# Kernel optimization log

Measured on AMD Instinct MI355X. Metric: run time of the kernel, lower is better.

The kernel has to match this reference:

```python
import jax, jax.numpy as jnp
import numpy as np

HIDDEN = 1024
OUT = 16

def setup_inputs() -> dict:
    key = jax.random.key(0)
    ks = jax.random.split(key, 12)
    bs, hl, hf = 256, 256, 32
    T, ad = 64, 16
    flat = hl * hf
    s = lambda fi, fo: 1.0 / np.sqrt(fi)
    return {
        "history": jax.random.normal(ks[0], (bs, hl, hf), jnp.float32),
        "action": jax.random.normal(ks[1], (bs, T, ad), jnp.float32),
        # carry-init Dense layers (c and h)
        "Wc": jax.random.normal(ks[2], (flat, HIDDEN), jnp.float32) * s(flat, HIDDEN),
        "bc": jnp.zeros((HIDDEN,), jnp.float32),
        "Wh": jax.random.normal(ks[3], (flat, HIDDEN), jnp.float32) * s(flat, HIDDEN),
        "bh": jnp.zeros((HIDDEN,), jnp.float32),
        # LSTM cell: gates ordered [i, f, g, o]; input dense has no bias (flax LSTMCell)
        "Wi": jax.random.normal(ks[4], (ad, 4 * HIDDEN), jnp.float32) * s(ad, HIDDEN),
        "Wr": jax.random.normal(ks[5], (HIDDEN, 4 * HIDDEN), jnp.float32) * s(HIDDEN, HIDDEN),
        "bg": jnp.zeros((4 * HIDDEN,), jnp.float32),
        # output projection
        "Wo": jax.random.normal(ks[6], (HIDDEN, OUT), jnp.float32) * s(HIDDEN, OUT),
        "bo": jnp.zeros((OUT,), jnp.float32),
    }


def reference(history, action, Wc, bc, Wh, bh, Wi, Wr, bg, Wo, bo):
    bs = history.shape[0]
    flat = history.reshape(bs, -1)
    c0 = jax.nn.relu(flat @ Wc + bc)  # [bs, H]
    h0 = jax.nn.relu(flat @ Wh + bh)  # [bs, H]

    # precompute input contribution to gates for all steps: [T, bs, 4H]
    xg = jnp.einsum('bta,ag->tbg', action, Wi)

    def step(carry, xg_t):
        c, h = carry
        g = xg_t + h @ Wr + bg  # [bs, 4H]
        i, f, gg, o = jnp.split(g, 4, axis=-1)
        c = jax.nn.sigmoid(f) * c + jax.nn.sigmoid(i) * jnp.tanh(gg)
        h = jax.nn.sigmoid(o) * jnp.tanh(c)
        return (c, h), h

    _, hs = jax.lax.scan(step, (c0, h0), xg)  # hs: [T, bs, H]
    x = jnp.transpose(hs, (1, 0, 2))  # [bs, T, H]
    # Dropout is deterministic (identity)
    return x @ Wo + bo  # [bs, T, OUT]
```

## Files before the change

### kernel.cpp

```cpp
#include <hip/hip_runtime.h>
#include <math.h>

#define BS      256
#define FLAT    8192
#define H       1024
#define G4      4096
#define T_STEPS 64
#define AD      16
#define NOUT    16

typedef __attribute__((ext_vector_type(8))) short    bf16x8;
typedef __attribute__((ext_vector_type(4))) float    f32x4;
typedef __attribute__((ext_vector_type(8))) unsigned short u16x8;
typedef __attribute__((ext_vector_type(4))) unsigned short u16x4;

__device__ __forceinline__ float sigf(float x) { return 1.0f / (1.0f + __expf(-x)); }
__device__ __forceinline__ float tanh_fast(float x) {
    float a = fabsf(x);
    float e = __expf(-2.0f * a);
    float r = (1.0f - e) / (1.0f + e);
    return copysignf(r, x);
}
__device__ __forceinline__ unsigned short f2bf(float x) {
    unsigned int u = __float_as_uint(x);
    unsigned int r = (u + 0x7FFFu + ((u >> 16) & 1u)) >> 16;
    return (unsigned short)r;
}
__device__ __forceinline__ float bf2f(unsigned short u) {
    return __uint_as_float(((unsigned int)u) << 16);
}

#define OFF_WRP  (1u<<20)
#define OFF_WIP  (OFF_WRP + (8u<<20))
#define OFF_BGP  (OFF_WIP + (256u<<10))
#define OFF_HPA  (OFF_BGP + (16u<<10))
#define OFF_HPB  (OFF_HPA + (512u<<10))
#define OFF_HS   (OFF_HPB + (512u<<10))
#define OFF_AHP  (OFF_HS + (32u<<20))
#define OFF_AXP  (OFF_AHP + (4u<<20))
#define OFF_PART (OFF_AXP + (1u<<20))

__global__ __launch_bounds__(256) void pack_wr(const float* __restrict__ Wr,
                                               unsigned short* __restrict__ Wp)
{
    int g  = blockIdx.x * 256 + threadIdx.x;
    int l  = g & 63;
    int nt = (g >> 6) & 3;
    int kc = (g >> 8) & 31;
    int nb = g >> 13;
    int col   = nt * 1024 + nb * 16 + (l & 15);
    int kbase = kc * 32 + (l >> 4) * 8;
    u16x8 o;
    #pragma unroll
    for (int i = 0; i < 8; ++i)
        o[i] = f2bf(Wr[(size_t)(kbase + i) * G4 + col]);
    *(u16x8*)&Wp[(size_t)g * 8] = o;
}

__global__ __launch_bounds__(256) void pack_wi(const float* __restrict__ Wi,
                                               unsigned short* __restrict__ Wp)
{
    int g  = blockIdx.x * 256 + threadIdx.x;
    int l  = g & 63;
    int nt = (g >> 6) & 3;
    int nb = g >> 8;
    int col   = nt * 1024 + nb * 16 + (l & 15);
    int kbase = (l >> 4) * 8;
    u16x8 o;
    #pragma unroll
    for (int i = 0; i < 8; ++i)
        o[i] = (kbase + i < AD) ? f2bf(Wi[(size_t)(kbase + i) * G4 + col]) : (unsigned short)0;
    *(u16x8*)&Wp[(size_t)g * 8] = o;
}

__global__ __launch_bounds__(256) void pack_bg(const float* __restrict__ bg,
                                               float* __restrict__ bgp)
{
    int t = blockIdx.x * 256 + threadIdx.x;
    int jj = t & 15, nt = (t >> 4) & 3, nb = t >> 6;
    bgp[t] = bg[nt * 1024 + nb * 16 + jj];
}

__global__ __launch_bounds__(256) void pack_hist(const float* __restrict__ hist,
                                                 unsigned short* __restrict__ Ap)
{
    int g  = blockIdx.x * 256 + threadIdx.x;
    int l  = g & 63;
    int kc = (g >> 6) & 255;
    int mb = g >> 14;
    const float* src = hist + (size_t)(mb * 16 + (l & 15)) * FLAT + kc * 32 + (l >> 4) * 8;
    float4 v0 = *(const float4*)src;
    float4 v1 = *(const float4*)(src + 4);
    u16x8 o;
    o[0]=f2bf(v0.x); o[1]=f2bf(v0.y); o[2]=f2bf(v0.z); o[3]=f2bf(v0.w);
    o[4]=f2bf(v1.x); o[5]=f2bf(v1.y); o[6]=f2bf(v1.z); o[7]=f2bf(v1.w);
    *(u16x8*)&Ap[(size_t)g * 8] = o;
}

__global__ __launch_bounds__(256) void pack_wb(const float* __restrict__ Wc,
                                               const float* __restrict__ Wh,
                                               unsigned short* __restrict__ Bp)
{
    int g  = blockIdx.x * 256 + threadIdx.x;
    int l  = g & 63;
    int kc = (g >> 6) & 255;
    int nb = g >> 14;
    const float* src = (nb & 64) ? Wh : Wc;
    int n = (nb & 63) * 16 + (l & 15);
    int k = kc * 32 + (l >> 4) * 8;
    u16x8 o;
    #pragma unroll
    for (int i = 0; i < 8; ++i)
        o[i] = f2bf(src[(size_t)(k + i) * H + n]);
    *(u16x8*)&Bp[(size_t)g * 8] = o;
}

__global__ __launch_bounds__(256) void pack_act(const float* __restrict__ act,
                                                unsigned short* __restrict__ Axp)
{
    int g = blockIdx.x * 256 + threadIdx.x;
    int l = g & 63;
    int q = (g >> 6) & 15;
    int t = g >> 10;
    int row = q * 16 + (l & 15);
    int kb  = (l >> 4) * 8;
    u16x8 o;
    if (kb < AD) {
        const float* src = act + ((size_t)row * T_STEPS + t) * AD + kb;
        float4 v0 = *(const float4*)src;
        float4 v1 = *(const float4*)(src + 4);
        o[0]=f2bf(v0.x); o[1]=f2bf(v0.y); o[2]=f2bf(v0.z); o[3]=f2bf(v0.w);
        o[4]=f2bf(v1.x); o[5]=f2bf(v1.y); o[6]=f2bf(v1.z); o[7]=f2bf(v1.w);
    } else {
        o = (u16x8){0,0,0,0,0,0,0,0};
    }
    *(u16x8*)&Axp[(size_t)g * 8] = o;
}

__global__ __launch_bounds__(256) void init_gemm_mfma(
    const unsigned short* __restrict__ Ap,
    const unsigned short* __restrict__ Bp,
    float* __restrict__ part)
{
    const int wg  = blockIdx.x;
    const int mb  = wg & 3;
    const int nbl = (wg >> 2) & 15;
    const int ks  = wg >> 6;
    const int tid = threadIdx.x;
    const int wv  = tid >> 6;
    const int l   = tid & 63;
    const int wm  = wv & 1;
    const int wn  = wv >> 1;

    const bf16x8* AV = (const bf16x8*)Ap;
    const bf16x8* BV = (const bf16x8*)Bp;
    const int am0 = mb * 4 + wm * 2;
    const int bn0 = nbl * 8 + wn * 4;
    const bf16x8* A0 = AV + (size_t)am0 * 16384 + l;
    const bf16x8* A1 = A0 + 16384;
    const bf16x8* B0 = BV + (size_t)bn0 * 16384 + l;
    const bf16x8* B1 = B0 + 16384;
    const bf16x8* B2 = B1 + 16384;
    const bf16x8* B3 = B2 + 16384;

    const int k0 = ks * 64;
    f32x4 acc[2][4];
    #pragma unroll
    for (int m = 0; m < 2; ++m)
        #pragma unroll
        for (int n = 0; n < 4; ++n)
            acc[m][n] = (f32x4){0.f, 0.f, 0.f, 0.f};

    bf16x8 a0 = A0[(size_t)k0 * 64], a1 = A1[(size_t)k0 * 64];
    bf16x8 b0 = B0[(size_t)k0 * 64], b1 = B1[(size_t)k0 * 64];
    bf16x8 b2 = B2[(size_t)k0 * 64], b3 = B3[(size_t)k0 * 64];

    for (int kc = k0; kc < k0 + 64; ++kc) {
        bf16x8 na0, na1, nb0, nb1, nb2, nb3;
        const bool more = (kc + 1) < k0 + 64;
        if (more) {
            size_t off = (size_t)(kc + 1) * 64;
            na0 = A0[off]; na1 = A1[off];
            nb0 = B0[off]; nb1 = B1[off]; nb2 = B2[off]; nb3 = B3[off];
        }
        acc[0][0] = __builtin_amdgcn_mfma_f32_16x16x32_bf16(a0, b0, acc[0][0], 0, 0, 0);
        acc[0][1] = __builtin_amdgcn_mfma_f32_16x16x32_bf16(a0, b1, acc[0][1], 0, 0, 0);
        acc[0][2] = __builtin_amdgcn_mfma_f32_16x16x32_bf16(a0, b2, acc[0][2], 0, 0, 0);
        acc[0][3] = __builtin_amdgcn_mfma_f32_16x16x32_bf16(a0, b3, acc[0][3], 0, 0, 0);
        acc[1][0] = __builtin_amdgcn_mfma_f32_16x16x32_bf16(a1, b0, acc[1][0], 0, 0, 0);
        acc[1][1] = __builtin_amdgcn_mfma_f32_16x16x32_bf16(a1, b1, acc[1][1], 0, 0, 0);
        acc[1][2] = __builtin_amdgcn_mfma_f32_16x16x32_bf16(a1, b2, acc[1][2], 0, 0, 0);
        acc[1][3] = __builtin_amdgcn_mfma_f32_16x16x32_bf16(a1, b3, acc[1][3], 0, 0, 0);
        if (more) { a0 = na0; a1 = na1; b0 = nb0; b1 = nb1; b2 = nb2; b3 = nb3; }
    }

    const int rbase = mb * 64 + wm * 32 + (l >> 4) * 4;
    const int cbase = nbl * 128 + wn * 64 + (l & 15);
    float* pdst = part + (size_t)ks * (BS * 2048);
    #pragma unroll
    for (int m = 0; m < 2; ++m)
        #pragma unroll
        for (int n = 0; n < 4; ++n)
            #pragma unroll
            for (int r = 0; r < 4; ++r)
                pdst[(size_t)(rbase + m * 16 + r) * 2048 + cbase + n * 16] = acc[m][n][r];
}

__global__ __launch_bounds__(256) void init_reduce(
    const float* __restrict__ part,
    const float* __restrict__ bc, const float* __restrict__ bh,
    float* __restrict__ cbuf, unsigned short* __restrict__ hp0)
{
    int e = blockIdx.x * 256 + threadIdx.x;
    int row = e >> 11, col = e & 2047;
    float s = (col < 1024) ? bc[col] : bh[col - 1024];
    #pragma unroll
    for (int ks = 0; ks < 4; ++ks)
        s += part[(size_t)ks * (BS * 2048) + e];
    s = fmaxf(s, 0.f);
    if (col < 1024) {
        cbuf[(size_t)row * H + col] = s;
    } else {
        int hid = col - 1024;
        int off = (row >> 6) * 65536 + (hid >> 5) * 2048 + ((row >> 4) & 3) * 512
                + ((((hid >> 3) & 3) << 4) + (row & 15)) * 8 + (hid & 7);
        hp0[off] = f2bf(s);
    }
}

__global__ __launch_bounds__(256) void lstm_step(
    const unsigned short* __restrict__ Axp,
    const unsigned short* __restrict__ Wip,
    const unsigned short* __restrict__ Wrp,
    const float* __restrict__ bgp,
    const unsigned short* __restrict__ Aprev,
    unsigned short* __restrict__ Anext,
    float* __restrict__ cbuf,
    unsigned short* __restrict__ hs_t,
    int t)
{
    __shared__ __align__(16) unsigned short sB[2][4096];

    const int tid = threadIdx.x;
    const int wg  = blockIdx.x;
    const int mb  = wg >> 6;
    const int nb  = wg & 63;
    const int wv  = tid >> 6;
    const int l   = tid & 63;

    const u16x8* Bsrc = (const u16x8*)(Wrp + (size_t)nb * 65536);
    {
        u16x8 s0 = Bsrc[tid], s1 = Bsrc[256 + tid];
        *(u16x8*)&sB[0][tid * 8]         = s0;
        *(u16x8*)&sB[0][(256 + tid) * 8] = s1;
    }
    u16x8 stg0 = Bsrc[512 + tid];
    u16x8 stg1 = Bsrc[768 + tid];

    const bf16x8* Asrc = ((const bf16x8*)Aprev) + mb * 8192 + wv * 64 + l;
    bf16x8 aE0 = Asrc[0],   aE1 = Asrc[256];
    bf16x8 aO0 = Asrc[512], aO1 = Asrc[768];

    f32x4 acc[4];
    {
        const bf16x8* WiB = ((const bf16x8*)Wip) + nb * 256;
        bf16x8 wb0 = WiB[0 * 64 + l], wb1 = WiB[1 * 64 + l],
               wb2 = WiB[2 * 64 + l], wb3 = WiB[3 * 64 + l];
        float g0 = bgp[nb * 64 +  0 + (l & 15)];
        float g1 = bgp[nb * 64 + 16 + (l & 15)];
        float g2 = bgp[nb * 64 + 32 + (l & 15)];
        float g3 = bgp[nb * 64 + 48 + (l & 15)];
        acc[0] = (f32x4){ g0, g0, g0, g0 };
        acc[1] = (f32x4){ g1, g1, g1, g1 };
        acc[2] = (f32x4){ g2, g2, g2, g2 };
        acc[3] = (f32x4){ g3, g3, g3, g3 };

        bf16x8 aa = *(((const bf16x8*)Axp) + ((size_t)t * 16 + mb * 4 + wv) * 64 + l);
        acc[0] = __builtin_amdgcn_mfma_f32_16x16x32_bf16(aa, wb0, acc[0], 0, 0, 0);
        acc[1] = __builtin_amdgcn_mfma_f32_16x16x32_bf16(aa, wb1, acc[1], 0, 0, 0);
        acc[2] = __builtin_amdgcn_mfma_f32_16x16x32_bf16(aa, wb2, acc[2], 0, 0, 0);
        acc[3] = __builtin_amdgcn_mfma_f32_16x16x32_bf16(aa, wb3, acc[3], 0, 0, 0);
    }
    __syncthreads();

    #define CHUNK_BODY(C, CB, AX0, AX1)                                             \
    {                                                                               \
        bf16x8 n0, n1;                                                              \
        if ((C) < 14) { n0 = Asrc[(2*(C)+4) * 256]; n1 = Asrc[(2*(C)+5) * 256]; }   \
        bf16x8 bf00 = *(const bf16x8*)&sB[CB][(0 * 64 + l) * 8];                    \
        bf16x8 bf01 = *(const bf16x8*)&sB[CB][(1 * 64 + l) * 8];                    \
        bf16x8 bf02 = *(const bf16x8*)&sB[CB][(2 * 64 + l) * 8];                    \
        bf16x8 bf03 = *(const bf16x8*)&sB[CB][(3 * 64 + l) * 8];                    \
        bf16x8 bf10 = *(const bf16x8*)&sB[CB][(4 * 64 + l) * 8];                    \
        bf16x8 bf11 = *(const bf16x8*)&sB[CB][(5 * 64 + l) * 8];                    \
        bf16x8 bf12 = *(const bf16x8*)&sB[CB][(6 * 64 + l) * 8];                    \
        bf16x8 bf13 = *(const bf16x8*)&sB[CB][(7 * 64 + l) * 8];                    \
        if ((C) < 15) {                                                             \
            *(u16x8*)&sB[(CB) ^ 1][tid * 8]         = stg0;                         \
            *(u16x8*)&sB[(CB) ^ 1][(256 + tid) * 8] = stg1;                         \
        }                                                                           \
        if ((C) < 14) {                                                             \
            stg0 = Bsrc[((C) + 2) * 512 + tid];                                     \
            stg1 = Bsrc[((C) + 2) * 512 + 256 + tid];                               \
        }                                                                           \
        acc[0] = __builtin_amdgcn_mfma_f32_16x16x32_bf16(AX0, bf00, acc[0], 0,0,0); \
        acc[1] = __builtin_amdgcn_mfma_f32_16x16x32_bf16(AX0, bf01, acc[1], 0,0,0); \
        acc[2] = __builtin_amdgcn_mfma_f32_16x16x32_bf16(AX0, bf02, acc[2], 0,0,0); \
        acc[3] = __builtin_amdgcn_mfma_f32_16x16x32_bf16(AX0, bf03, acc[3], 0,0,0); \
        acc[0] = __builtin_amdgcn_mfma_f32_16x16x32_bf16(AX1, bf10, acc[0], 0,0,0); \
        acc[1] = __builtin_amdgcn_mfma_f32_16x16x32_bf16(AX1, bf11, acc[1], 0,0,0); \
        acc[2] = __builtin_amdgcn_mfma_f32_16x16x32_bf16(AX1, bf12, acc[2], 0,0,0); \
        acc[3] = __builtin_amdgcn_mfma_f32_16x16x32_bf16(AX1, bf13, acc[3], 0,0,0); \
        if ((C) < 14) { AX0 = n0; AX1 = n1; }                                       \
        __syncthreads();                                                            \
    }

    for (int it = 0; it < 8; ++it) {
        const int c0 = 2 * it;
        CHUNK_BODY(c0,     0, aE0, aE1)
        CHUNK_BODY(c0 + 1, 1, aO0, aO1)
    }
    #undef CHUNK_BODY

    {
        const int jj   = l & 15;
        const int hid  = nb * 16 + jj;
        const int rowb = mb * 64 + wv * 16 + (l >> 4) * 4;
        const int kc   = nb >> 1;
        const int hgrp = ((nb & 1) << 1) | (jj >> 3);
        const int ii   = jj & 7;
        #pragma unroll
        for (int r = 0; r < 4; ++r) {
            int row = rowb + r;
            float gi = acc[0][r], gf = acc[1][r], gg = acc[2][r], go = acc[3][r];
            size_t off = (size_t)row * H + hid;
            float cv = sigf(gf) * cbuf[off] + sigf(gi) * tanh_fast(gg);
            cbuf[off] = cv;
            float hv = sigf(go) * tanh_fast(cv);
            unsigned short hb = f2bf(hv);
            hs_t[off] = hb;
            size_t poff = (size_t)mb * 65536 + kc * 2048 + wv * 512
                        + (hgrp * 16 + (row & 15)) * 8 + ii;
            Anext[poff] = hb;
        }
    }
}

__global__ __launch_bounds__(256) void out_proj(
    const unsigned short* __restrict__ hs,
    const float* __restrict__ Wo,
    const float* __restrict__ bo,
    float* __restrict__ out)
{
    __shared__ float sWo[H * NOUT];
    const int tid = threadIdx.x;
    for (int idx = tid; idx < H * NOUT; idx += 256) sWo[idx] = Wo[idx];
    __syncthreads();

    const int o  = tid & 15;
    const int pl = tid >> 4;
    const float bias = bo[o];
    #pragma unroll
    for (int pass = 0; pass < 4; ++pass) {
        const int pair = blockIdx.x * 64 + pass * 16 + pl;
        const int b = pair >> 6;
        const int t = pair & 63;
        const unsigned short* hrow = hs + ((size_t)t * BS + b) * H;
        float acc = bias;
        for (int k = 0; k < H; k += 8) {
            u16x8 u = *(const u16x8*)&hrow[k];
            #pragma unroll
            for (int j = 0; j < 8; ++j)
                acc = fmaf(bf2f(u[j]), sWo[(k + j) * 16 + o], acc);
        }
        out[(size_t)pair * 16 + o] = acc;
    }
}

extern "C" void kernel_launch(void* const* d_in, const int* in_sizes, int n_in,
                              void* d_out, int out_size, void* d_ws, size_t ws_size,
                              hipStream_t stream)
{
    const float* hist = (const float*)d_in[0];
    const float* act  = (const float*)d_in[1];
    const float* Wc   = (const float*)d_in[2];
    const float* bc   = (const float*)d_in[3];
    const float* Wh   = (const float*)d_in[4];
    const float* bh   = (const float*)d_in[5];
    const float* Wi   = (const float*)d_in[6];
    const float* Wr   = (const float*)d_in[7];
    const float* bg   = (const float*)d_in[8];
    const float* Wo   = (const float*)d_in[9];
    const float* bo   = (const float*)d_in[10];
    float* out = (float*)d_out;

    char* W = (char*)d_ws;
    float*          cbuf = (float*)W;
    unsigned short* Wrp  = (unsigned short*)(W + OFF_WRP);
    unsigned short* Wip  = (unsigned short*)(W + OFF_WIP);
    float*          bgp  = (float*)(W + OFF_BGP);
    unsigned short* hpA  = (unsigned short*)(W + OFF_HPA);
    unsigned short* hpB  = (unsigned short*)(W + OFF_HPB);
    unsigned short* hs   = (unsigned short*)(W + OFF_HS);
    unsigned short* Bwp  = (unsigned short*)(W + OFF_HS);
    unsigned short* Ahp  = (unsigned short*)(W + OFF_AHP);
    unsigned short* Axp  = (unsigned short*)(W + OFF_AXP);
    float*          part = (float*)(W + OFF_PART);

    pack_wr  <<<dim3(2048), dim3(256), 0, stream>>>(Wr, Wrp);
    pack_wi  <<<dim3(64),   dim3(256), 0, stream>>>(Wi, Wip);
    pack_bg  <<<dim3(16),   dim3(256), 0, stream>>>(bg, bgp);
    pack_hist<<<dim3(1024), dim3(256), 0, stream>>>(hist, Ahp);
    pack_wb  <<<dim3(8192), dim3(256), 0, stream>>>(Wc, Wh, Bwp);
    pack_act <<<dim3(256),  dim3(256), 0, stream>>>(act, Axp);

    init_gemm_mfma<<<dim3(256), dim3(256), 0, stream>>>(Ahp, Bwp, part);
    init_reduce  <<<dim3(2048), dim3(256), 0, stream>>>(part, bc, bh, cbuf, hpA);

    for (int t = 0; t < T_STEPS; ++t) {
        const unsigned short* Ap = (t & 1) ? hpB : hpA;
        unsigned short*       An = (t & 1) ? hpA : hpB;
        lstm_step<<<dim3(256), dim3(256), 0, stream>>>(
            Axp, Wip, Wrp, bgp, Ap, An, cbuf, hs + (size_t)t * BS * H, t);
    }

    out_proj<<<dim3(256), dim3(256), 0, stream>>>(hs, Wo, bo, out);
}
```

Before: 729.5 us.

## Fuse LSTM steps into persistent kernel with grid barrier and MFMA output projection

Replaces 64 per-step kernel launches with one persistent kernel of 256 workgroups that loops over time steps. Steps are separated by an atomic grid barrier, and the cell state stays in registers across steps. The output projection is rewritten to use bf16 MFMA with a packed Wo instead of scalar FMAs. This removes per-step launch overhead and the cbuf global round-trips. In exchange it depends on all 256 blocks being co-resident, and the spin barrier adds its own latency.

```diff
diff --git a/kernel.cpp b/kernel.cpp
--- a/kernel.cpp
+++ b/kernel.cpp
@@ -12,7 +12,6 @@
 typedef __attribute__((ext_vector_type(8))) short    bf16x8;
 typedef __attribute__((ext_vector_type(4))) float    f32x4;
 typedef __attribute__((ext_vector_type(8))) unsigned short u16x8;
-typedef __attribute__((ext_vector_type(4))) unsigned short u16x4;
 
 __device__ __forceinline__ float sigf(float x) { return 1.0f / (1.0f + __expf(-x)); }
 __device__ __forceinline__ float tanh_fast(float x) {
@@ -25,9 +24,6 @@
     unsigned int u = __float_as_uint(x);
     unsigned int r = (u + 0x7FFFu + ((u >> 16) & 1u)) >> 16;
     return (unsigned short)r;
-}
-__device__ __forceinline__ float bf2f(unsigned short u) {
-    return __uint_as_float(((unsigned int)u) << 16);
 }
 
 #define OFF_WRP  (1u<<20)
@@ -39,6 +35,8 @@
 #define OFF_AHP  (OFF_HS + (32u<<20))
 #define OFF_AXP  (OFF_AHP + (4u<<20))
 #define OFF_PART (OFF_AXP + (1u<<20))
+#define OFF_WOP  (OFF_PART + (8u<<20))
+#define OFF_BAR  (OFF_WOP + (64u<<10))
 
 __global__ __launch_bounds__(256) void pack_wr(const float* __restrict__ Wr,
                                                unsigned short* __restrict__ Wp)
@@ -135,6 +133,23 @@
         o = (u16x8){0,0,0,0,0,0,0,0};
     }
     *(u16x8*)&Axp[(size_t)g * 8] = o;
+}
+
+__global__ __launch_bounds__(256) void pack_wo(const float* __restrict__ Wo,
+                                               unsigned short* __restrict__ Wop)
+{
+    int g = blockIdx.x * 256 + threadIdx.x;
+    int l = g & 63;
+    int kc = g >> 6;
+    u16x8 o;
+    #pragma unroll
+    for (int i = 0; i < 8; ++i)
+        o[i] = f2bf(Wo[(size_t)(kc * 32 + (l >> 4) * 8 + i) * NOUT + (l & 15)]);
+    *(u16x8*)&Wop[(size_t)g * 8] = o;
+}
+
+__global__ void bar_init(unsigned int* bar) {
+    if (threadIdx.x == 0 && blockIdx.x == 0) *bar = 0u;
 }
 
 __global__ __launch_bounds__(256) void init_gemm_mfma(
@@ -228,16 +243,16 @@
     }
 }
 
-__global__ __launch_bounds__(256) void lstm_step(
+__global__ __launch_bounds__(256) void lstm_scan_persist(
     const unsigned short* __restrict__ Axp,
     const unsigned short* __restrict__ Wip,
     const unsigned short* __restrict__ Wrp,
     const float* __restrict__ bgp,
-    const unsigned short* __restrict__ Aprev,
-    unsigned short* __restrict__ Anext,
-    float* __restrict__ cbuf,
-    unsigned short* __restrict__ hs_t,
-    int t)
+    const float* __restrict__ cbuf,
+    unsigned short* __restrict__ hpA,
+    unsigned short* __restrict__ hpB,
+    unsigned short* __restrict__ hs,
+    unsigned int*   __restrict__ bar)
 {
     __shared__ __align__(16) unsigned short sB[2][4096];
 
@@ -248,133 +263,169 @@
     const int wv  = tid >> 6;
     const int l   = tid & 63;
 
+    const int jj   = l & 15;
+    const int hid  = nb * 16 + jj;
+    const int rowb = mb * 64 + wv * 16 + (l >> 4) * 4;
+    const int kcp  = nb >> 1;
+    const int hgrp = ((nb & 1) << 1) | (jj >> 3);
+    const int ii   = jj & 7;
+
+    float c_reg[4];
+    #pragma unroll
+    for (int r = 0; r < 4; ++r)
+        c_reg[r] = cbuf[(size_t)(rowb + r) * H + hid];
+
+    const bf16x8* WiB = ((const bf16x8*)Wip) + nb * 256;
+    const bf16x8 wb0 = WiB[0 * 64 + l], wb1 = WiB[1 * 64 + l],
+                 wb2 = WiB[2 * 64 + l], wb3 = WiB[3 * 64 + l];
+    const float g0 = bgp[nb * 64 +  0 + jj];
+    const float g1 = bgp[nb * 64 + 16 + jj];
+    const float g2 = bgp[nb * 64 + 32 + jj];
+    const float g3 = bgp[nb * 64 + 48 + jj];
+
     const u16x8* Bsrc = (const u16x8*)(Wrp + (size_t)nb * 65536);
-    {
-        u16x8 s0 = Bsrc[tid], s1 = Bsrc[256 + tid];
-        *(u16x8*)&sB[0][tid * 8]         = s0;
-        *(u16x8*)&sB[0][(256 + tid) * 8] = s1;
-    }
-    u16x8 stg0 = Bsrc[512 + tid];
-    u16x8 stg1 = Bsrc[768 + tid];
-
-    const bf16x8* Asrc = ((const bf16x8*)Aprev) + mb * 8192 + wv * 64 + l;
-    bf16x8 aE0 = Asrc[0],   aE1 = Asrc[256];
-    bf16x8 aO0 = Asrc[512], aO1 = Asrc[768];
-
-    f32x4 acc[4];
-    {
-        const bf16x8* WiB = ((const bf16x8*)Wip) + nb * 256;
-        bf16x8 wb0 = WiB[0 * 64 + l], wb1 = WiB[1 * 64 + l],
-               wb2 = WiB[2 * 64 + l], wb3 = WiB[3 * 64 + l];
-        float g0 = bgp[nb * 64 +  0 + (l & 15)];
-        float g1 = bgp[nb * 64 + 16 + (l & 15)];
-        float g2 = bgp[nb * 64 + 32 + (l & 15)];
-        float g3 = bgp[nb * 64 + 48 + (l & 15)];
+
+    #pragma unroll 1
+    for (int t = 0; t < T_STEPS; ++t) {
+        const unsigned short* Ap = (t & 1) ? hpB : hpA;
+        unsigned short*       An = (t & 1) ? hpA : hpB;
+        unsigned short*       hs_t = hs + (size_t)t * (BS * H);
+
+        {
+            u16x8 s0 = Bsrc[tid], s1 = Bsrc[256 + tid];
+            *(u16x8*)&sB[0][tid * 8]         = s0;
+            *(u16x8*)&sB[0][(256 + tid) * 8] = s1;
+        }
+        u16x8 stg0 = Bsrc[512 + tid];
+        u16x8 stg1 = Bsrc[768 + tid];
+
+        const bf16x8* Asrc = ((const bf16x8*)Ap) + mb * 8192 + wv * 64 + l;
+        bf16x8 aE0 = Asrc[0],   aE1 = Asrc[256];
+        bf16x8 aO0 = Asrc[512], aO1 = Asrc[768];
+
+        f32x4 acc[4];
         acc[0] = (f32x4){ g0, g0, g0, g0 };
         acc[1] = (f32x4){ g1, g1, g1, g1 };
         acc[2] = (f32x4){ g2, g2, g2, g2 };
         acc[3] = (f32x4){ g3, g3, g3, g3 };
-
-        bf16x8 aa = *(((const bf16x8*)Axp) + ((size_t)t * 16 + mb * 4 + wv) * 64 + l);
-        acc[0] = __builtin_amdgcn_mfma_f32_16x16x32_bf16(aa, wb0, acc[0], 0, 0, 0);
-        acc[1] = __builtin_amdgcn_mfma_f32_16x16x32_bf16(aa, wb1, acc[1], 0, 0, 0);
-        acc[2] = __builtin_amdgcn_mfma_f32_16x16x32_bf16(aa, wb2, acc[2], 0, 0, 0);
-        acc[3] = __builtin_amdgcn_mfma_f32_16x16x32_bf16(aa, wb3, acc[3], 0, 0, 0);
-    }
-    __syncthreads();
-
-    #define CHUNK_BODY(C, CB, AX0, AX1)                                             \
-    {                                                                               \
-        bf16x8 n0, n1;                                                              \
-        if ((C) < 14) { n0 = Asrc[(2*(C)+4) * 256]; n1 = Asrc[(2*(C)+5) * 256]; }   \
-        bf16x8 bf00 = *(const bf16x8*)&sB[CB][(0 * 64 + l) * 8];                    \
-        bf16x8 bf01 = *(const bf16x8*)&sB[CB][(1 * 64 + l) * 8];                    \
-        bf16x8 bf02 = *(const bf16x8*)&sB[CB][(2 * 64 + l) * 8];                    \
-        bf16x8 bf03 = *(const bf16x8*)&sB[CB][(3 * 64 + l) * 8];                    \
-        bf16x8 bf10 = *(const bf16x8*)&sB[CB][(4 * 64 + l) * 8];                    \
-        bf16x8 bf11 = *(const bf16x8*)&sB[CB][(5 * 64 + l) * 8];                    \
-        bf16x8 bf12 = *(const bf16x8*)&sB[CB][(6 * 64 + l) * 8];                    \
-        bf16x8 bf13 = *(const bf16x8*)&sB[CB][(7 * 64 + l) * 8];                    \
-        if ((C) < 15) {                                                             \
-            *(u16x8*)&sB[(CB) ^ 1][tid * 8]         = stg0;                         \
-            *(u16x8*)&sB[(CB) ^ 1][(256 + tid) * 8] = stg1;                         \
-        }                                                                           \
-        if ((C) < 14) {                                                             \
-            stg0 = Bsrc[((C) + 2) * 512 + tid];                                     \
-            stg1 = Bsrc[((C) + 2) * 512 + 256 + tid];                               \
-        }                                                                           \
-        acc[0] = __builtin_amdgcn_mfma_f32_16x16x32_bf16(AX0, bf00, acc[0], 0,0,0); \
-        acc[1] = __builtin_amdgcn_mfma_f32_16x16x32_bf16(AX0, bf01, acc[1], 0,0,0); \
-        acc[2] = __builtin_amdgcn_mfma_f32_16x16x32_bf16(AX0, bf02, acc[2], 0,0,0); \
-        acc[3] = __builtin_amdgcn_mfma_f32_16x16x32_bf16(AX0, bf03, acc[3], 0,0,0); \
-        acc[0] = __builtin_amdgcn_mfma_f32_16x16x32_bf16(AX1, bf10, acc[0], 0,0,0); \
-        acc[1] = __builtin_amdgcn_mfma_f32_16x16x32_bf16(AX1, bf11, acc[1], 0,0,0); \
-        acc[2] = __builtin_amdgcn_mfma_f32_16x16x32_bf16(AX1, bf12, acc[2], 0,0,0); \
-        acc[3] = __builtin_amdgcn_mfma_f32_16x16x32_bf16(AX1, bf13, acc[3], 0,0,0); \
-        if ((C) < 14) { AX0 = n0; AX1 = n1; }                                       \
-        __syncthreads();                                                            \
-    }
-
-    for (int it = 0; it < 8; ++it) {
-        const int c0 = 2 * it;
-        CHUNK_BODY(c0,     0, aE0, aE1)
-        CHUNK_BODY(c0 + 1, 1, aO0, aO1)
-    }
-    #undef CHUNK_BODY
-
-    {
-        const int jj   = l & 15;
-        const int hid  = nb * 16 + jj;
-        const int rowb = mb * 64 + wv * 16 + (l >> 4) * 4;
-        const int kc   = nb >> 1;
-        const int hgrp = ((nb & 1) << 1) | (jj >> 3);
-        const int ii   = jj & 7;
+        {
+            bf16x8 aa = *(((const bf16x8*)Axp) + ((size_t)t * 16 + mb * 4 + wv) * 64 + l);
+            acc[0] = __builtin_amdgcn_mfma_f32_16x16x32_bf16(aa, wb0, acc[0], 0, 0, 0);
+            acc[1] = __builtin_amdgcn_mfma_f32_16x16x32_bf16(aa, wb1, acc[1], 0, 0, 0);
+            acc[2] = __builtin_amdgcn_mfma_f32_16x16x32_bf16(aa, wb2, acc[2], 0, 0, 0);
+            acc[3] = __builtin_amdgcn_mfma_f32_16x16x32_bf16(aa, wb3, acc[3], 0, 0, 0);
+        }
+        __syncthreads();
+
+        #define CHUNK_BODY(C, CB, AX0, AX1)                                             \
+        {                                                                               \
+            bf16x8 n0, n1;                                                              \
+            if ((C) < 14) { n0 = Asrc[(2*(C)+4) * 256]; n1 = Asrc[(2*(C)+5) * 256]; }   \
+            bf16x8 bf00 = *(const bf16x8*)&sB[CB][(0 * 64 + l) * 8];                    \
+            bf16x8 bf01 = *(const bf16x8*)&sB[CB][(1 * 64 + l) * 8];                    \
+            bf16x8 bf02 = *(const bf16x8*)&sB[CB][(2 * 64 + l) * 8];                    \
+            bf16x8 bf03 = *(const bf16x8*)&sB[CB][(3 * 64 + l) * 8];                    \
+            bf16x8 bf10 = *(const bf16x8*)&sB[CB][(4 * 64 + l) * 8];                    \
+            bf16x8 bf11 = *(const bf16x8*)&sB[CB][(5 * 64 + l) * 8];                    \
+            bf16x8 bf12 = *(const bf16x8*)&sB[CB][(6 * 64 + l) * 8];                    \
+            bf16x8 bf13 = *(const bf16x8*)&sB[CB][(7 * 64 + l) * 8];                    \
+            if ((C) < 15) {                                                             \
+                *(u16x8*)&sB[(CB) ^ 1][tid * 8]         = stg0;                         \
+                *(u16x8*)&sB[(CB) ^ 1][(256 + tid) * 8] = stg1;                         \
+            }                                                                           \
+            if ((C) < 14) {                                                             \
+                stg0 = Bsrc[((C) + 2) * 512 + tid];                                     \
+                stg1 = Bsrc[((C) + 2) * 512 + 256 + tid];                               \
+            }                                                                           \
+            acc[0] = __builtin_amdgcn_mfma_f32_16x16x32_bf16(AX0, bf00, acc[0], 0,0,0); \
+            acc[1] = __builtin_amdgcn_mfma_f32_16x16x32_bf16(AX0, bf01, acc[1], 0,0,0); \
+            acc[2] = __builtin_amdgcn_mfma_f32_16x16x32_bf16(AX0, bf02, acc[2], 0,0,0); \
+            acc[3] = __builtin_amdgcn_mfma_f32_16x16x32_bf16(AX0, bf03, acc[3], 0,0,0); \
+            acc[0] = __builtin_amdgcn_mfma_f32_16x16x32_bf16(AX1, bf10, acc[0], 0,0,0); \
+            acc[1] = __builtin_amdgcn_mfma_f32_16x16x32_bf16(AX1, bf11, acc[1], 0,0,0); \
+            acc[2] = __builtin_amdgcn_mfma_f32_16x16x32_bf16(AX1, bf12, acc[2], 0,0,0); \
+            acc[3] = __builtin_amdgcn_mfma_f32_16x16x32_bf16(AX1, bf13, acc[3], 0,0,0); \
+            if ((C) < 14) { AX0 = n0; AX1 = n1; }                                       \
+            __syncthreads();                                                            \
+        }
+
+        for (int it = 0; it < 8; ++it) {
+            const int c0 = 2 * it;
+            CHUNK_BODY(c0,     0, aE0, aE1)
+            CHUNK_BODY(c0 + 1, 1, aO0, aO1)
+        }
+        #undef CHUNK_BODY
+
         #pragma unroll
         for (int r = 0; r < 4; ++r) {
             int row = rowb + r;
             float gi = acc[0][r], gf = acc[1][r], gg = acc[2][r], go = acc[3][r];
-            size_t off = (size_t)row * H + hid;
-            float cv = sigf(gf) * cbuf[off] + sigf(gi) * tanh_fast(gg);
-            cbuf[off] = cv;
+            float cv = sigf(gf) * c_reg[r] + sigf(gi) * tanh_fast(gg);
+            c_reg[r] = cv;
             float hv = sigf(go) * tanh_fast(cv);
             unsigned short hb = f2bf(hv);
-            hs_t[off] = hb;
-            size_t poff = (size_t)mb * 65536 + kc * 2048 + wv * 512
+            hs_t[(size_t)row * H + hid] = hb;
+            size_t poff = (size_t)mb * 65536 + kcp * 2048 + wv * 512
                         + (hgrp * 16 + (row & 15)) * 8 + ii;
-            Anext[poff] = hb;
-        }
-    }
-}
-
-__global__ __launch_bounds__(256) void out_proj(
+            An[poff] = hb;
+        }
+
+        if (t < T_STEPS - 1) {
+            __syncthreads();
+            if (tid == 0) {
+                __hip_atomic_fetch_add(bar, 1u, __ATOMIC_RELEASE,
+                                       __HIP_MEMORY_SCOPE_AGENT);
+                const unsigned int target = 256u * (unsigned int)(t + 1);
+                while (__hip_atomic_load(bar, __ATOMIC_ACQUIRE,
+                                         __HIP_MEMORY_SCOPE_AGENT) < target) {
+                    __builtin_amdgcn_s_sleep(1);
+                }
+            }
+            __syncthreads();
+            __builtin_amdgcn_fence(__ATOMIC_ACQUIRE, "agent");
+        }
+    }
+}
+
+__global__ __launch_bounds__(256) void out_gemm(
     const unsigned short* __restrict__ hs,
-    const float* __restrict__ Wo,
+    const unsigned short* __restrict__ Wop,
     const float* __restrict__ bo,
     float* __restrict__ out)
 {
-    __shared__ float sWo[H * NOUT];
+    __shared__ __align__(16) unsigned short sWo[32 * 64 * 8];
     const int tid = threadIdx.x;
-    for (int idx = tid; idx < H * NOUT; idx += 256) sWo[idx] = Wo[idx];
+    #pragma unroll
+    for (int u = 0; u < 8; ++u) {
+        int idx = u * 256 + tid;
+        *(u16x8*)&sWo[idx * 8] = ((const u16x8*)Wop)[idx];
+    }
     __syncthreads();
 
-    const int o  = tid & 15;
-    const int pl = tid >> 4;
-    const float bias = bo[o];
-    #pragma unroll
-    for (int pass = 0; pass < 4; ++pass) {
-        const int pair = blockIdx.x * 64 + pass * 16 + pl;
-        const int b = pair >> 6;
-        const int t = pair & 63;
-        const unsigned short* hrow = hs + ((size_t)t * BS + b) * H;
-        float acc = bias;
-        for (int k = 0; k < H; k += 8) {
-            u16x8 u = *(const u16x8*)&hrow[k];
-            #pragma unroll
-            for (int j = 0; j < 8; ++j)
-                acc = fmaf(bf2f(u[j]), sWo[(k + j) * 16 + o], acc);
-        }
-        out[(size_t)pair * 16 + o] = acc;
-    }
+    const int wv = tid >> 6;
+    const int l  = tid & 63;
+    const int m  = blockIdx.x * 4 + wv;
+    const int b  = m >> 2;
+    const int t0 = (m & 3) * 16;
+
+    const unsigned short* Arow =
+        hs + ((size_t)(t0 + (l & 15)) * BS + b) * H + (l >> 4) * 8;
+
+    f32x4 acc = (f32x4){0.f, 0.f, 0.f, 0.f};
+    bf16x8 a = *(const bf16x8*)Arow;
+    for (int kc = 0; kc < 32; ++kc) {
+        bf16x8 an;
+        if (kc < 31) an = *(const bf16x8*)(Arow + (kc + 1) * 32);
+        bf16x8 w = *(const bf16x8*)&sWo[(kc * 64 + l) * 8];
+        acc = __builtin_amdgcn_mfma_f32_16x16x32_bf16(a, w, acc, 0, 0, 0);
+        if (kc < 31) a = an;
+    }
+
+    const float bias = bo[l & 15];
+    const int p0 = m * 16 + (l >> 4) * 4;
+    #pragma unroll
+    for (int r = 0; r < 4; ++r)
+        out[(size_t)(p0 + r) * NOUT + (l & 15)] = acc[r] + bias;
 }
 
 extern "C" void kernel_launch(void* const* d_in, const int* in_sizes, int n_in,
@@ -406,23 +457,23 @@
     unsigned short* Ahp  = (unsigned short*)(W + OFF_AHP);
     unsigned short* Axp  = (unsigned short*)(W + OFF_AXP);
     float*          part = (float*)(W + OFF_PART);
-
+    unsigned short* Wop  = (unsigned short*)(W + OFF_WOP);
+    unsigned int*   bar  = (unsigned int*)(W + OFF_BAR);
+
+    bar_init <<<dim3(1),    dim3(64),  0, stream>>>(bar);
     pack_wr  <<<dim3(2048), dim3(256), 0, stream>>>(Wr, Wrp);
     pack_wi  <<<dim3(64),   dim3(256), 0, stream>>>(Wi, Wip);
     pack_bg  <<<dim3(16),   dim3(256), 0, stream>>>(bg, bgp);
     pack_hist<<<dim3(1024), dim3(256), 0, stream>>>(hist, Ahp);
     pack_wb  <<<dim3(8192), dim3(256), 0, stream>>>(Wc, Wh, Bwp);
     pack_act <<<dim3(256),  dim3(256), 0, stream>>>(act, Axp);
+    pack_wo  <<<dim3(8),    dim3(256), 0, stream>>>(Wo, Wop);
 
     init_gemm_mfma<<<dim3(256), dim3(256), 0, stream>>>(Ahp, Bwp, part);
     init_reduce  <<<dim3(2048), dim3(256), 0, stream>>>(part, bc, bh, cbuf, hpA);
 
-    for (int t = 0; t < T_STEPS; ++t) {
-        const unsigned short* Ap = (t & 1) ? hpB : hpA;
-        unsigned short*       An = (t & 1) ? hpA : hpB;
-        lstm_step<<<dim3(256), dim3(256), 0, stream>>>(
-            Axp, Wip, Wrp, bgp, Ap, An, cbuf, hs + (size_t)t * BS * H, t);
-    }
-
-    out_proj<<<dim3(256), dim3(256), 0, stream>>>(hs, Wo, bo, out);
-}
+    lstm_scan_persist<<<dim3(256), dim3(256), 0, stream>>>(
+        Axp, Wip, Wrp, bgp, cbuf, hpA, hpB, hs, bar);
+
+    out_gemm<<<dim3(256), dim3(256), 0, stream>>>(hs, Wop, bo, out);
+}
```

Result: slower. 2.212 ms (+203.3%).
